# Optimization experiments

Hardware: AMD Instinct MI355X
Metric: run time of the kernel (lower is better)

The kernel has to match this reference:

```python
import jax, jax.numpy as jnp
import numpy as np

EMB_SIZE = 1_000_000
EMB_DIM = 64
B = 16384
K = 20


def setup_inputs() -> dict:
    key = jax.random.key(0)
    k1, k2, k3, k4, k5, k6 = jax.random.split(key, 6)
    initrange = 0.5 / EMB_DIM
    return {
        "pos_u": jax.random.randint(k1, (B,), 0, EMB_SIZE),
        "pos_v": jax.random.randint(k2, (B,), 0, EMB_SIZE),
        "neg_u": jax.random.randint(k3, (B, K), 0, EMB_SIZE),
        "neg_v": jax.random.randint(k4, (B, K), 0, EMB_SIZE),
        # u_embeddings ~ U(-initrange, initrange); v_embeddings is zero-init in the
        # original but we use small random values so gradients are non-trivial.
        "u_emb": jax.random.uniform(k5, (EMB_SIZE, EMB_DIM), jnp.float32, -initrange, initrange),
        "v_emb": jax.random.uniform(k6, (EMB_SIZE, EMB_DIM), jnp.float32, -initrange, initrange),
    }


def reference(pos_u, pos_v, neg_u, neg_v, u_emb, v_emb):
    # Positive edges: [B, D] gathers, dot along D.
    pos_score = jnp.sum(u_emb[pos_u] * v_emb[pos_v], axis=-1)          # [B]
    # Negative edges: [B, K, D] gathers.
    neg_score = jnp.sum(u_emb[neg_u] * v_emb[neg_v], axis=-1)          # [B, K]
    # Original applies logsigmoid(score) for BOTH positive and negative edges
    # and sums -logsigmoid over all of them.
    loss = -jax.nn.log_sigmoid(pos_score) - jnp.sum(jax.nn.log_sigmoid(neg_score), axis=-1)
    return jnp.sum(loss)
```

## Files before the change

### kernel.cpp

```cpp
#include <hip/hip_runtime.h>


constexpr int Bn = 16384;
constexpr int Kn = 20;
constexpr int Dn = 64;
constexpr int NPAIRS = Bn * (Kn + 1);

#define BDIM 256
#define NBLOCKS 2048

__global__ __launch_bounds__(BDIM) void w2v_partial(
    const int* __restrict__ pos_u, const int* __restrict__ pos_v,
    const int* __restrict__ neg_u, const int* __restrict__ neg_v,
    const float* __restrict__ u_emb, const float* __restrict__ v_emb,
    float* __restrict__ partials)
{
    const int lane16 = threadIdx.x & 15;
    const int group  = (blockIdx.x * BDIM + threadIdx.x) >> 4;
    const int ngroups = (NBLOCKS * BDIM) >> 4;

    float acc = 0.f;
    for (int p = group; p < NPAIRS; p += ngroups) {
        int iu, iv;
        if (p < Bn) { iu = pos_u[p];      iv = pos_v[p]; }
        else        { iu = neg_u[p - Bn]; iv = neg_v[p - Bn]; }

        const float4 a = *reinterpret_cast<const float4*>(u_emb + (size_t)iu * Dn + (lane16 << 2));
        const float4 b = *reinterpret_cast<const float4*>(v_emb + (size_t)iv * Dn + (lane16 << 2));
        float s = a.x*b.x + a.y*b.y + a.z*b.z + a.w*b.w;

        s += __shfl_xor(s, 1);
        s += __shfl_xor(s, 2);
        s += __shfl_xor(s, 4);
        s += __shfl_xor(s, 8);

        if (lane16 == 0) {
            float y = -s;
            acc += fmaxf(y, 0.f) + log1pf(expf(-fabsf(y)));
        }
    }

    acc += __shfl_xor(acc, 16);
    acc += __shfl_xor(acc, 32);

    __shared__ float red[BDIM / 64];
    if ((threadIdx.x & 63) == 0) red[threadIdx.x >> 6] = acc;
    __syncthreads();
    if (threadIdx.x == 0)
        partials[blockIdx.x] = red[0] + red[1] + red[2] + red[3];
}

__global__ __launch_bounds__(BDIM) void w2v_reduce(
    const float* __restrict__ partials, float* __restrict__ out)
{
    float s = 0.f;
    for (int i = threadIdx.x; i < NBLOCKS; i += BDIM) s += partials[i];
    s += __shfl_xor(s, 1);
    s += __shfl_xor(s, 2);
    s += __shfl_xor(s, 4);
    s += __shfl_xor(s, 8);
    s += __shfl_xor(s, 16);
    s += __shfl_xor(s, 32);
    __shared__ float red[BDIM / 64];
    if ((threadIdx.x & 63) == 0) red[threadIdx.x >> 6] = s;
    __syncthreads();
    if (threadIdx.x == 0) out[0] = red[0] + red[1] + red[2] + red[3];
}

extern "C" void kernel_launch(void* const* d_in, const int* in_sizes, int n_in,
                              void* d_out, int out_size, void* d_ws, size_t ws_size,
                              hipStream_t stream) {
    const int*   pos_u = (const int*)d_in[0];
    const int*   pos_v = (const int*)d_in[1];
    const int*   neg_u = (const int*)d_in[2];
    const int*   neg_v = (const int*)d_in[3];
    const float* u_emb = (const float*)d_in[4];
    const float* v_emb = (const float*)d_in[5];
    float* out = (float*)d_out;
    float* partials = (float*)d_ws;

    w2v_partial<<<NBLOCKS, BDIM, 0, stream>>>(pos_u, pos_v, neg_u, neg_v,
                                              u_emb, v_emb, partials);
    w2v_reduce<<<1, BDIM, 0, stream>>>(partials, out);
}
```

Before: 36.98 us.

## Fuse final reduction via last-block atomic counter and unroll gather loop by two

Replaces the separate single-block reduce kernel with a last-block-done pattern: each block publishes its partial, increments an atomic counter, and the final block sums all partials and writes the output. The main loop is also unrolled by two so each 16-lane group has two independent pairs of embedding gathers in flight. This targets the second kernel launch cost and memory latency in the gather, but adds a memsetAsync per call and atomic traffic.

```diff
diff --git a/kernel.cpp b/kernel.cpp
--- a/kernel.cpp
+++ b/kernel.cpp
@@ -8,63 +8,101 @@
 
 #define BDIM 256
 #define NBLOCKS 2048
+#define NGROUPS ((NBLOCKS * BDIM) >> 4)
 
-__global__ __launch_bounds__(BDIM) void w2v_partial(
+__device__ __forceinline__ void pair_idx(
+    int p, const int* __restrict__ pu, const int* __restrict__ pv,
+    const int* __restrict__ nu, const int* __restrict__ nv, int& iu, int& iv)
+{
+    if (p < Bn) { iu = pu[p];      iv = pv[p]; }
+    else        { iu = nu[p - Bn]; iv = nv[p - Bn]; }
+}
+
+__device__ __forceinline__ float softplus_neg(float s) {
+    float y = -s;
+    return fmaxf(y, 0.f) + log1pf(expf(-fabsf(y)));
+}
+
+__device__ __forceinline__ float red16(float s) {
+    s += __shfl_xor(s, 1);
+    s += __shfl_xor(s, 2);
+    s += __shfl_xor(s, 4);
+    s += __shfl_xor(s, 8);
+    return s;
+}
+
+__global__ __launch_bounds__(BDIM) void w2v_fused(
     const int* __restrict__ pos_u, const int* __restrict__ pos_v,
     const int* __restrict__ neg_u, const int* __restrict__ neg_v,
     const float* __restrict__ u_emb, const float* __restrict__ v_emb,
-    float* __restrict__ partials)
+    float* __restrict__ partials, unsigned int* __restrict__ counter,
+    float* __restrict__ out)
 {
     const int lane16 = threadIdx.x & 15;
     const int group  = (blockIdx.x * BDIM + threadIdx.x) >> 4;
-    const int ngroups = (NBLOCKS * BDIM) >> 4;
+    const int doff   = lane16 << 2;
 
     float acc = 0.f;
-    for (int p = group; p < NPAIRS; p += ngroups) {
+    int p = group;
+    for (; p + NGROUPS < NPAIRS; p += 2 * NGROUPS) {
+        int iu0, iv0, iu1, iv1;
+        pair_idx(p,           pos_u, pos_v, neg_u, neg_v, iu0, iv0);
+        pair_idx(p + NGROUPS, pos_u, pos_v, neg_u, neg_v, iu1, iv1);
+
+        const float4 a0 = *reinterpret_cast<const float4*>(u_emb + (size_t)iu0 * Dn + doff);
+        const float4 b0 = *reinterpret_cast<const float4*>(v_emb + (size_t)iv0 * Dn + doff);
+        const float4 a1 = *reinterpret_cast<const float4*>(u_emb + (size_t)iu1 * Dn + doff);
+        const float4 b1 = *reinterpret_cast<const float4*>(v_emb + (size_t)iv1 * Dn + doff);
+
+        float s0 = a0.x*b0.x + a0.y*b0.y + a0.z*b0.z + a0.w*b0.w;
+        float s1 = a1.x*b1.x + a1.y*b1.y + a1.z*b1.z + a1.w*b1.w;
+        s0 = red16(s0);
+        s1 = red16(s1);
+        if (lane16 == 0) acc += softplus_neg(s0) + softplus_neg(s1);
+    }
+    if (p < NPAIRS) {
         int iu, iv;
-        if (p < Bn) { iu = pos_u[p];      iv = pos_v[p]; }
-        else        { iu = neg_u[p - Bn]; iv = neg_v[p - Bn]; }
+        pair_idx(p, pos_u, pos_v, neg_u, neg_v, iu, iv);
+        const float4 a = *reinterpret_cast<const float4*>(u_emb + (size_t)iu * Dn + doff);
+        const float4 b = *reinterpret_cast<const float4*>(v_emb + (size_t)iv * Dn + doff);
+        float s = a.x*b.x + a.y*b.y + a.z*b.z + a.w*b.w;
+        s = red16(s);
+        if (lane16 == 0) acc += softplus_neg(s);
+    }
 
-        const float4 a = *reinterpret_cast<const float4*>(u_emb + (size_t)iu * Dn + (lane16 << 2));
-        const float4 b = *reinterpret_cast<const float4*>(v_emb + (size_t)iv * Dn + (lane16 << 2));
-        float s = a.x*b.x + a.y*b.y + a.z*b.z + a.w*b.w;
+    acc += __shfl_xor(acc, 16);
+    acc += __shfl_xor(acc, 32);
+    __shared__ float red[BDIM / 64];
+    if ((threadIdx.x & 63) == 0) red[threadIdx.x >> 6] = acc;
+    __syncthreads();
 
+    __shared__ bool is_last;
+    if (threadIdx.x == 0) {
+        float bsum = red[0] + red[1] + red[2] + red[3];
+        __hip_atomic_store(&partials[blockIdx.x], bsum, __ATOMIC_RELAXED,
+                           __HIP_MEMORY_SCOPE_AGENT);
+        unsigned t = __hip_atomic_fetch_add(counter, 1u, __ATOMIC_ACQ_REL,
+                                            __HIP_MEMORY_SCOPE_AGENT);
+        is_last = (t == NBLOCKS - 1);
+    }
+    __syncthreads();
+
+    if (is_last) {
+        float s = 0.f;
+        for (int i = threadIdx.x; i < NBLOCKS; i += BDIM)
+            s += __hip_atomic_load(&partials[i], __ATOMIC_RELAXED,
+                                   __HIP_MEMORY_SCOPE_AGENT);
         s += __shfl_xor(s, 1);
         s += __shfl_xor(s, 2);
         s += __shfl_xor(s, 4);
         s += __shfl_xor(s, 8);
-
-        if (lane16 == 0) {
-            float y = -s;
-            acc += fmaxf(y, 0.f) + log1pf(expf(-fabsf(y)));
-        }
+        s += __shfl_xor(s, 16);
+        s += __shfl_xor(s, 32);
+        __shared__ float red2[BDIM / 64];
+        if ((threadIdx.x & 63) == 0) red2[threadIdx.x >> 6] = s;
+        __syncthreads();
+        if (threadIdx.x == 0) out[0] = red2[0] + red2[1] + red2[2] + red2[3];
     }
-
-    acc += __shfl_xor(acc, 16);
-    acc += __shfl_xor(acc, 32);
-
-    __shared__ float red[BDIM / 64];
-    if ((threadIdx.x & 63) == 0) red[threadIdx.x >> 6] = acc;
-    __syncthreads();
-    if (threadIdx.x == 0)
-        partials[blockIdx.x] = red[0] + red[1] + red[2] + red[3];
-}
-
-__global__ __launch_bounds__(BDIM) void w2v_reduce(
-    const float* __restrict__ partials, float* __restrict__ out)
-{
-    float s = 0.f;
-    for (int i = threadIdx.x; i < NBLOCKS; i += BDIM) s += partials[i];
-    s += __shfl_xor(s, 1);
-    s += __shfl_xor(s, 2);
-    s += __shfl_xor(s, 4);
-    s += __shfl_xor(s, 8);
-    s += __shfl_xor(s, 16);
-    s += __shfl_xor(s, 32);
-    __shared__ float red[BDIM / 64];
-    if ((threadIdx.x & 63) == 0) red[threadIdx.x >> 6] = s;
-    __syncthreads();
-    if (threadIdx.x == 0) out[0] = red[0] + red[1] + red[2] + red[3];
 }
 
 extern "C" void kernel_launch(void* const* d_in, const int* in_sizes, int n_in,
@@ -77,9 +115,12 @@
     const float* u_emb = (const float*)d_in[4];
     const float* v_emb = (const float*)d_in[5];
     float* out = (float*)d_out;
-    float* partials = (float*)d_ws;
 
-    w2v_partial<<<NBLOCKS, BDIM, 0, stream>>>(pos_u, pos_v, neg_u, neg_v,
-                                              u_emb, v_emb, partials);
-    w2v_reduce<<<1, BDIM, 0, stream>>>(partials, out);
+    unsigned int* counter  = (unsigned int*)d_ws;
+    float*        partials = (float*)((char*)d_ws + 256);
+
+    hipMemsetAsync(d_ws, 0, sizeof(unsigned int), stream);
+
+    w2v_fused<<<NBLOCKS, BDIM, 0, stream>>>(pos_u, pos_v, neg_u, neg_v,
+                                            u_emb, v_emb, partials, counter, out);
 }
```

After: 99.10 us. +168.0%, slower.
